# Performance work log

Hardware: AMD Instinct MI355X
Metric: run time of the kernel (lower is better)

## Reference

```python
import jax, jax.numpy as jnp
import numpy as np

B, CQ, CK, CV, CO = 16, 256, 256, 256, 256
H, W = 80, 80          # query spatial size (P3-like)
KH, KW = 40, 40        # key/value spatial size (P4-like)
HEADS = 4
R2 = 2 * 2             # region_size ** 2
SCALE = 1.0 / np.float32(np.sqrt(CQ))


def conv1x1(x, w, b):
    # 1x1 conv == per-pixel linear map over channels
    return jnp.einsum('bchw,oc->bohw', x, w) + b[None, :, None, None]


def setup_inputs() -> dict:
    key = jax.random.key(0)
    ks = jax.random.split(key, 10)
    s = 0.05
    return {
        'query': jax.random.normal(ks[0], (B, CQ, H, W), jnp.float32),
        'key':   jax.random.normal(ks[1], (B, CK, KH, KW), jnp.float32),
        'wq': jax.random.normal(ks[2], (CQ, CQ), jnp.float32) * s,
        'bq': jax.random.normal(ks[3], (CQ,), jnp.float32) * s,
        'wk': jax.random.normal(ks[4], (CK, CK), jnp.float32) * s,
        'bk': jax.random.normal(ks[5], (CK,), jnp.float32) * s,
        'wv': jax.random.normal(ks[6], (CV, CV), jnp.float32) * s,
        'bv': jax.random.normal(ks[7], (CV,), jnp.float32) * s,
        'wo': jax.random.normal(ks[8], (CO, CV), jnp.float32) * s,
        'bo': jax.random.normal(ks[9], (CO,), jnp.float32) * s,
    }


def reference(query, key, wq, bq, wk, bk, wv, bv, wo, bo):
    # value defaults to key in the original module
    q = conv1x1(query, wq, bq)               # [B,CQ,H,W]
    k = conv1x1(key, wk, bk)                 # [B,CK,KH,KW]
    v = conv1x1(key, wv, bv)                 # [B,CV,KH,KW]

    b, cq, h, w = q.shape
    # All R2 'patches' in the source are the SAME interpolation (no offsets),
    # so compute it once; bilinear resize matches torch align_corners=False.
    ki = jax.image.resize(k, (b, k.shape[1], h, w), method='bilinear')
    vi = jax.image.resize(v, (b, v.shape[1], h, w), method='bilinear')

    q5 = q.reshape(b, HEADS, cq // HEADS, h, w)
    k5 = ki.reshape(b, HEADS, k.shape[1] // HEADS, h, w)
    v5 = vi.reshape(b, HEADS, v.shape[1] // HEADS, h, w)

    # per-region score; identical for every region patch
    score = jnp.einsum('bhcxy,bhcxy->bhxy', q5, k5) * SCALE     # [B,h,H,W]
    scores = jnp.broadcast_to(score[:, :, None], (b, HEADS, R2, h, w))
    # NOTE: original uses nn.Softmax(dim=3) -> normalizes over the H axis
    attn = jax.nn.softmax(scores, axis=3)                       # [B,h,R2,H,W]

    # out = sum over regions of attn * v (v identical across regions)
    out = jnp.einsum('bhrxy,bhcxy->bhcxy', attn, v5)            # [B,h,C/h,H,W]
    out = out.reshape(b, -1, h, w)                              # [B,CV,H,W]
    return conv1x1(out, wo, bo)                                 # [B,CO,H,W]
```

## Files before the change

### kernel.cpp

```cpp
#include <hip/hip_runtime.h>
#include <hip/hip_bf16.h>

typedef __bf16 bf16;
typedef __attribute__((ext_vector_type(4))) float f32x4;
typedef __attribute__((ext_vector_type(8))) __bf16 bf16x8;
typedef __attribute__((ext_vector_type(4))) __bf16 bf16x4;

static __device__ __forceinline__ void gl16(const void* g, void* l) {
  __builtin_amdgcn_global_load_lds((const __attribute__((address_space(1))) void*)g,
                                   (__attribute__((address_space(3))) void*)l, 16, 0, 0);
}
static __device__ __forceinline__ bf16x8 frag(const bf16* tile, int row, int kb) {
  return *(const bf16x8*)(tile + row * 64 + ((((kb) >> 3) ^ (row & 7)) << 3));
}

__global__ void wpre(const float* __restrict__ w0, const float* __restrict__ w1,
                     const float* __restrict__ w2, const float* __restrict__ w3,
                     bf16* __restrict__ dst) {
  const float* srcs[4] = {w0, w1, w2, w3};
  const float* s = srcs[blockIdx.y];
  bf16* d = dst + (size_t)blockIdx.y * 65536;
  int base = blockIdx.x * 2048 + threadIdx.x * 8;
  f32x4 a = *(const f32x4*)(s + base);
  f32x4 b = *(const f32x4*)(s + base + 4);
  bf16x8 v = {(bf16)a[0], (bf16)a[1], (bf16)a[2], (bf16)a[3],
              (bf16)b[0], (bf16)b[1], (bf16)b[2], (bf16)b[3]};
  *(bf16x8*)(d + base) = v;
}

__global__ __launch_bounds__(256, 3)
void qscore(const float* __restrict__ query, const bf16* __restrict__ Wq,
            const float* __restrict__ bq, const bf16* __restrict__ Kpm,
            float* __restrict__ score) {
  __shared__ alignas(16) char smem[64 * 264 * 2];
  const int t = threadIdx.x;
  const int b = blockIdx.z;
  const int p0 = blockIdx.x * 64;
  const int w = t >> 6, l = t & 63;
  const int lrow = l & 15, ksel = l >> 4;
  const int pq = t & 15, cq = t >> 4;
  const float* actb = query + (size_t)b * 256 * 6400;

  auto Bt = [&](int buf) { return (bf16*)(smem + buf * 8192); };

  f32x4 Ar[4];
  auto ALOAD = [&](int kt) {
    const int k0 = kt * 64;
#pragma unroll
    for (int j = 0; j < 4; ++j)
      Ar[j] = *(const f32x4*)(actb + (size_t)(k0 + cq * 4 + j) * 6400 + p0 + pq * 4);
  };
  auto ASTORE = [&](int buf) {
    bf16* tile = Bt(buf);
#pragma unroll
    for (int e = 0; e < 4; ++e) {
      int row = pq * 4 + e;
      bf16x4 v = {(bf16)Ar[0][e], (bf16)Ar[1][e], (bf16)Ar[2][e], (bf16)Ar[3][e]};
      *(bf16x4*)(tile + row * 64 + ((((cq >> 1) ^ (row & 7)) << 3) | ((cq & 1) << 2))) = v;
    }
  };

  f32x4 acc[4][4];
#pragma unroll
  for (int i = 0; i < 4; ++i)
#pragma unroll
    for (int j = 0; j < 4; ++j) acc[i][j] = (f32x4){0.f, 0.f, 0.f, 0.f};

  auto COMPUTE = [&](int kt, int buf) {
    const int k0 = kt * 64;
    bf16x8 af[4][2];
#pragma unroll
    for (int mi = 0; mi < 4; ++mi)
#pragma unroll
      for (int kk = 0; kk < 2; ++kk)
        af[mi][kk] = *(const bf16x8*)(Wq + (size_t)(w * 64 + mi * 16 + lrow) * 256 +
                                      k0 + kk * 32 + ksel * 8);
    bf16x8 bv[4][2];
#pragma unroll
    for (int ni = 0; ni < 4; ++ni)
#pragma unroll
      for (int kk = 0; kk < 2; ++kk)
        bv[ni][kk] = frag(Bt(buf), ni * 16 + lrow, kk * 32 + ksel * 8);
#pragma unroll
    for (int kk = 0; kk < 2; ++kk)
#pragma unroll
      for (int mi = 0; mi < 4; ++mi)
#pragma unroll
        for (int ni = 0; ni < 4; ++ni)
          acc[mi][ni] = __builtin_amdgcn_mfma_f32_16x16x32_bf16(af[mi][kk], bv[ni][kk],
                                                                acc[mi][ni], 0, 0, 0);
  };

  ALOAD(0);
  ASTORE(0);
  __syncthreads();
#pragma unroll
  for (int kt = 0; kt < 4; ++kt) {
    if (kt < 3) ALOAD(kt + 1);
    COMPUTE(kt, kt & 1);
    if (kt < 3) ASTORE((kt + 1) & 1);
    __syncthreads();
  }

  __syncthreads();
  bf16* Qs = (bf16*)smem;
#pragma unroll
  for (int mi = 0; mi < 4; ++mi) {
#pragma unroll
    for (int r = 0; r < 4; ++r) {
      int o = w * 64 + mi * 16 + ksel * 4 + r;
      float bvf = bq[o];
#pragma unroll
      for (int ni = 0; ni < 4; ++ni) {
        int px = ni * 16 + lrow;
        Qs[px * 264 + o] = (bf16)(acc[mi][ni][r] + bvf);
      }
    }
  }
  __syncthreads();

  {
    int pl = t & 63, hd = t >> 6;
    int p = p0 + pl;
    int x = p / 80, y = p % 80;
    float cx = 0.5f * x - 0.25f;
    int ix = (int)floorf(cx);
    float wx1 = cx - ix;
    int x0 = ix < 0 ? 0 : ix, x1 = (ix + 1 > 39) ? 39 : ix + 1;
    float cy = 0.5f * y - 0.25f;
    int iy = (int)floorf(cy);
    float wy1 = cy - iy;
    int y0 = iy < 0 ? 0 : iy, y1 = (iy + 1 > 39) ? 39 : iy + 1;
    float w00 = (1.f - wx1) * (1.f - wy1), w01 = (1.f - wx1) * wy1;
    float w10 = wx1 * (1.f - wy1), w11 = wx1 * wy1;
    const bf16* k00 = Kpm + ((size_t)b * 1600 + x0 * 40 + y0) * 256 + hd * 64;
    const bf16* k01 = Kpm + ((size_t)b * 1600 + x0 * 40 + y1) * 256 + hd * 64;
    const bf16* k10 = Kpm + ((size_t)b * 1600 + x1 * 40 + y0) * 256 + hd * 64;
    const bf16* k11 = Kpm + ((size_t)b * 1600 + x1 * 40 + y1) * 256 + hd * 64;
    float dot = 0.f;
#pragma unroll
    for (int i = 0; i < 8; ++i) {
      bf16x8 qv = *(const bf16x8*)(Qs + pl * 264 + hd * 64 + i * 8);
      bf16x8 a = *(const bf16x8*)(k00 + i * 8);
      bf16x8 c = *(const bf16x8*)(k01 + i * 8);
      bf16x8 d = *(const bf16x8*)(k10 + i * 8);
      bf16x8 e = *(const bf16x8*)(k11 + i * 8);
#pragma unroll
      for (int j = 0; j < 8; ++j) {
        float kup = w00 * (float)a[j] + w01 * (float)c[j] + w10 * (float)d[j] + w11 * (float)e[j];
        dot += (float)qv[j] * kup;
      }
    }
    score[((size_t)b * 4 + hd) * 6400 + p] = dot * 0.0625f;
  }
}

__global__ __launch_bounds__(512, 1)
void kv_gemm(const float* __restrict__ key,
             const bf16* __restrict__ Wk, const float* __restrict__ bk, bf16* __restrict__ Kpm,
             const bf16* __restrict__ Wv, const float* __restrict__ bv, bf16* __restrict__ Vpm) {
  __shared__ alignas(16) char smem[65536];
  const int P = 1600;
  const int t = threadIdx.x;
  const int b = blockIdx.z;
  const int m0 = blockIdx.x * 128;
  const int sel = blockIdx.y >> 1;
  const int n0 = (blockIdx.y & 1) * 128;
  const bf16* W = sel ? Wv : Wk;
  const float* bias = sel ? bv : bk;
  bf16* out = sel ? Vpm : Kpm;
  const int w = t >> 6, l = t & 63;
  const int wr = w & 1, wc = w >> 1;
  const int lrow = l & 15, koff = (l >> 4) * 8;
  const int up = t & 31, uk = t >> 5;
  const float* actb = key + (size_t)b * 256 * P;

  f32x4 Ar[4];
  f32x4 acc[4][2];
#pragma unroll
  for (int i = 0; i < 4; ++i)
#pragma unroll
    for (int j = 0; j < 2; ++j) acc[i][j] = (f32x4){0.f, 0.f, 0.f, 0.f};

  auto Ab = [&](int buf) { return (bf16*)(smem + buf * 16384); };
  auto Bb = [&](int buf) { return (bf16*)(smem + 32768 + buf * 16384); };

  auto GLOADB = [&](int kt, int buf) {
    const int k0 = kt * 64;
#pragma unroll
    for (int call = 0; call < 2; ++call) {
      int idx = call * 512 + t;
      int row = idx >> 3, u = idx & 7;
      gl16(W + (size_t)(n0 + row) * 256 + k0 + ((u ^ (row & 7)) << 3), Bb(buf) + idx * 8);
    }
  };
  auto ALOAD = [&](int kt) {
    const int k0 = kt * 64;
    int ps = m0 + up * 4;
    if (ps > P - 4) ps = P - 4;
#pragma unroll
    for (int j = 0; j < 4; ++j)
      Ar[j] = *(const f32x4*)(actb + (size_t)(k0 + uk * 4 + j) * P + ps);
  };
  auto ASTORE = [&](int buf) {
#pragma unroll
    for (int j = 0; j < 4; ++j) {
      int row = up * 4 + j;
      int cs = (uk * 4) ^ ((row & 7) << 3);
      bf16x4 v = {(bf16)Ar[0][j], (bf16)Ar[1][j], (bf16)Ar[2][j], (bf16)Ar[3][j]};
      *(bf16x4*)(Ab(buf) + row * 64 + cs) = v;
    }
  };
  auto COMPUTE = [&](int buf) {
#pragma unroll
    for (int kk = 0; kk < 2; ++kk) {
      bf16x8 af[4], bvv[2];
      const int kb = kk * 32 + koff;
#pragma unroll
      for (int i = 0; i < 4; ++i) af[i] = frag(Ab(buf), wr * 64 + i * 16 + lrow, kb);
#pragma unroll
      for (int j = 0; j < 2; ++j) bvv[j] = frag(Bb(buf), wc * 32 + j * 16 + lrow, kb);
#pragma unroll
      for (int i = 0; i < 4; ++i)
#pragma unroll
        for (int j = 0; j < 2; ++j)
          acc[i][j] = __builtin_amdgcn_mfma_f32_16x16x32_bf16(af[i], bvv[j], acc[i][j], 0, 0, 0);
    }
  };

  GLOADB(0, 0);
  ALOAD(0);
  ASTORE(0);
  __syncthreads();
#pragma unroll
  for (int kt = 0; kt < 4; ++kt) {
    const int cur = kt & 1;
    if (kt < 3) { GLOADB(kt + 1, cur ^ 1); ALOAD(kt + 1); }
    __builtin_amdgcn_sched_barrier(0);
    COMPUTE(cur);
    if (kt < 3) ASTORE(cur ^ 1);
    __syncthreads();
  }

  bf16* Sc = (bf16*)smem;
#pragma unroll
  for (int mi = 0; mi < 4; ++mi) {
#pragma unroll
    for (int ni = 0; ni < 2; ++ni) {
      int ch = wc * 32 + ni * 16 + (l & 15);
      float bvf = bias[n0 + ch];
#pragma unroll
      for (int r = 0; r < 4; ++r) {
        int p = wr * 64 + mi * 16 + (l >> 4) * 4 + r;
        Sc[p * 136 + ch] = (bf16)(acc[mi][ni][r] + bvf);
      }
    }
  }
  __syncthreads();
  bf16* ob = out + (size_t)b * P * 256;
#pragma unroll
  for (int pass = 0; pass < 4; ++pass) {
    int unit = pass * 512 + t;
    int row = unit >> 4, cu = unit & 15;
    if (m0 + row < P) {
      bf16x8 v = *(const bf16x8*)(Sc + row * 136 + cu * 8);
      *(bf16x8*)(ob + (size_t)(m0 + row) * 256 + n0 + cu * 8) = v;
    }
  }
}

__global__ void smax_kernel(float* __restrict__ score) {
  __shared__ float s[6400];
  const int hd = blockIdx.x, b = blockIdx.y, t = threadIdx.x;
  float* buf = score + ((size_t)b * 4 + hd) * 6400;
  for (int i = t; i < 6400; i += 256) s[i] = buf[i];
  __syncthreads();
  if (t < 80) {
    const int y = t;
    float m = -1e30f;
    for (int x = 0; x < 80; ++x) m = fmaxf(m, s[x * 80 + y]);
    float sum = 0.f;
    for (int x = 0; x < 80; ++x) {
      float e = __expf(s[x * 80 + y] - m);
      s[x * 80 + y] = e;
      sum += e;
    }
    float inv = 4.0f / sum;
    for (int x = 0; x < 80; ++x) buf[x * 80 + y] = s[x * 80 + y] * inv;
  }
}

__global__ __launch_bounds__(256, 4)
void uv_gemm(const bf16* __restrict__ Vpm, const bf16* __restrict__ Wo,
             bf16* __restrict__ Uv) {
  __shared__ alignas(16) bf16 Vt[64 * 64];
  const int t = threadIdx.x;
  const int b = blockIdx.z;
  const int hd = blockIdx.y;
  const int q0 = blockIdx.x * 64;
  const int w = t >> 6, l = t & 63;
  const int lrow = l & 15, ksel = l >> 4;

  const bf16* vsrc = Vpm + ((size_t)b * 1600 + q0) * 256 + hd * 64;
#pragma unroll
  for (int call = 0; call < 2; ++call) {
    int idx = (w * 2 + call) * 64 + l;
    int q = idx >> 3, u = idx & 7;
    gl16(vsrc + (size_t)q * 256 + ((u ^ (q & 7)) << 3), Vt + idx * 8);
  }
  asm volatile("s_waitcnt vmcnt(0)" ::: "memory");
  __syncthreads();

  f32x4 acc[4][4];
#pragma unroll
  for (int i = 0; i < 4; ++i)
#pragma unroll
    for (int j = 0; j < 4; ++j) acc[i][j] = (f32x4){0.f, 0.f, 0.f, 0.f};

#pragma unroll
  for (int kk = 0; kk < 2; ++kk) {
    bf16x8 af[4], bv[4];
#pragma unroll
    for (int mi = 0; mi < 4; ++mi)
      af[mi] = *(const bf16x8*)(Wo + (size_t)(w * 64 + mi * 16 + lrow) * 256 +
                                hd * 64 + kk * 32 + ksel * 8);
#pragma unroll
    for (int ni = 0; ni < 4; ++ni)
      bv[ni] = frag(Vt, ni * 16 + lrow, kk * 32 + ksel * 8);
#pragma unroll
    for (int mi = 0; mi < 4; ++mi)
#pragma unroll
      for (int ni = 0; ni < 4; ++ni)
        acc[mi][ni] = __builtin_amdgcn_mfma_f32_16x16x32_bf16(af[mi], bv[ni], acc[mi][ni], 0, 0, 0);
  }

  bf16* ob = Uv + ((size_t)(b * 4 + hd)) * 256 * 1600;
#pragma unroll
  for (int mi = 0; mi < 4; ++mi) {
#pragma unroll
    for (int ni = 0; ni < 4; ++ni) {
#pragma unroll
      for (int r = 0; r < 4; ++r) {
        int o = w * 64 + mi * 16 + ksel * 4 + r;
        int q = q0 + ni * 16 + lrow;
        ob[(size_t)o * 1600 + q] = (bf16)acc[mi][ni][r];
      }
    }
  }
}

__global__ __launch_bounds__(256, 8)
void combine(const bf16* __restrict__ Uv, const float* __restrict__ attn,
             const float* __restrict__ bo, float* __restrict__ out) {
  __shared__ bf16 Us[4][1600];
  __shared__ int   sx0[80], sx1[80];
  __shared__ float swx[80];
  const int t = threadIdx.x;
  const int o = blockIdx.x;
  const int b = blockIdx.y;

  const bf16* usrc = Uv + (size_t)(b * 4) * 256 * 1600 + (size_t)o * 1600;
  for (int idx = t; idx < 800; idx += 256) {
    int hd = idx / 200, u = idx % 200;
    *(bf16x8*)&Us[hd][u * 8] = *(const bf16x8*)(usrc + (size_t)hd * 256 * 1600 + u * 8);
  }
  if (t < 80) {
    float c = 0.5f * t - 0.25f;
    int i0 = (int)floorf(c);
    swx[t] = c - i0;
    sx0[t] = i0 < 0 ? 0 : i0;
    sx1[t] = (i0 + 1 > 39) ? 39 : i0 + 1;
  }
  __syncthreads();

  const float bias = bo[o];
  const float* attb = attn + (size_t)b * 4 * 6400;
  float* op = out + ((size_t)b * 256 + o) * 6400;

  for (int p = t; p < 6400; p += 256) {
    int x = p / 80, y = p - x * 80;
    int x0 = sx0[x], x1 = sx1[x], y0 = sx0[y], y1 = sx1[y];
    float wx1 = swx[x], wy1 = swx[y];
    float w00 = (1.f - wx1) * (1.f - wy1), w01 = (1.f - wx1) * wy1;
    float w10 = wx1 * (1.f - wy1), w11 = wx1 * wy1;
    int q00 = x0 * 40 + y0, q01 = x0 * 40 + y1, q10 = x1 * 40 + y0, q11 = x1 * 40 + y1;
    float acc = bias;
#pragma unroll
    for (int hd = 0; hd < 4; ++hd) {
      float up = w00 * (float)Us[hd][q00] + w01 * (float)Us[hd][q01] +
                 w10 * (float)Us[hd][q10] + w11 * (float)Us[hd][q11];
      acc += attb[hd * 6400 + p] * up;
    }
    op[p] = acc;
  }
}

extern "C" void kernel_launch(void* const* d_in, const int* in_sizes, int n_in,
                              void* d_out, int out_size, void* d_ws, size_t ws_size,
                              hipStream_t stream) {
  const float* query = (const float*)d_in[0];
  const float* key   = (const float*)d_in[1];
  const float* wq    = (const float*)d_in[2];
  const float* bq    = (const float*)d_in[3];
  const float* wk    = (const float*)d_in[4];
  const float* bk    = (const float*)d_in[5];
  const float* wv    = (const float*)d_in[6];
  const float* bv    = (const float*)d_in[7];
  const float* wo    = (const float*)d_in[8];
  const float* bo    = (const float*)d_in[9];

  char* ws = (char*)d_ws;
  bf16*  Uv    = (bf16*)(ws);
  bf16*  Kpm   = (bf16*)(ws + 52428800);
  bf16*  Vpm   = (bf16*)(ws + 65536000);
  float* score = (float*)(ws + 78643200);
  bf16*  Wb    = (bf16*)(ws + 85196800);
  bf16* wqb = Wb, *wkb = Wb + 65536, *wvb = Wb + 131072, *wob = Wb + 196608;

  wpre<<<dim3(32, 4), 256, 0, stream>>>(wq, wk, wv, wo, Wb);
  kv_gemm<<<dim3(13, 4, 16), 512, 0, stream>>>(key, wkb, bk, Kpm, wvb, bv, Vpm);
  qscore<<<dim3(100, 1, 16), 256, 0, stream>>>(query, wqb, bq, Kpm, score);
  smax_kernel<<<dim3(4, 16), 256, 0, stream>>>(score);
  uv_gemm<<<dim3(25, 4, 16), 256, 0, stream>>>(Vpm, wob, Uv);
  combine<<<dim3(256, 16), 256, 0, stream>>>(Uv, score, bo, (float*)d_out);
}
```

Measured before the change: 170.6 us.

## Pre-transpose query and key to pixel-major bf16 for direct-to-LDS GEMM loads

Adds a transpose kernel that converts the fp32 channel-major query and key tensors into pixel-major bf16 buffers in scratch space (query into the Uv workspace region, key into the output buffer). The qscore and kv_gemm kernels then stage their activation tiles with asynchronous global-to-LDS 16-byte loads instead of register loads, conversion and swizzled LDS stores. This takes the conversion and scatter work out of the GEMM main loops, at the cost of two extra launches and an extra write and read of the activations. Reusing the output and Uv buffers as scratch depends on later kernels overwriting them in the right order.

```diff
diff --git a/kernel.cpp b/kernel.cpp
--- a/kernel.cpp
+++ b/kernel.cpp
@@ -28,8 +28,40 @@
   *(bf16x8*)(d + base) = v;
 }
 
+__global__ __launch_bounds__(256, 4)
+void tpose(const float* __restrict__ src, bf16* __restrict__ dst, int P) {
+  __shared__ bf16 tile[400][40];
+  const int t = threadIdx.x;
+  const int p0 = blockIdx.x * 400;
+  const int k0 = blockIdx.y * 32;
+  const int b = blockIdx.z;
+  const float* s = src + (size_t)b * 256 * P + (size_t)k0 * P + p0;
+  bf16* d = dst + (size_t)b * P * 256 + (size_t)p0 * 256 + k0;
+
+#pragma unroll
+  for (int pass = 0; pass < 13; ++pass) {
+    int idx = pass * 256 + t;
+    if (idx < 3200) {
+      int r = idx / 100, sg = idx - r * 100;
+      f32x4 v = *(const f32x4*)(s + (size_t)r * P + sg * 4);
+#pragma unroll
+      for (int j = 0; j < 4; ++j) tile[sg * 4 + j][r] = (bf16)v[j];
+    }
+  }
+  __syncthreads();
+#pragma unroll
+  for (int pass = 0; pass < 7; ++pass) {
+    int idx = pass * 256 + t;
+    if (idx < 1600) {
+      int row = idx >> 2, u = idx & 3;
+      bf16x8 v = *(const bf16x8*)&tile[row][u * 8];
+      *(bf16x8*)(d + (size_t)row * 256 + u * 8) = v;
+    }
+  }
+}
+
 __global__ __launch_bounds__(256, 3)
-void qscore(const float* __restrict__ query, const bf16* __restrict__ Wq,
+void qscore(const bf16* __restrict__ Qraw, const bf16* __restrict__ Wq,
             const float* __restrict__ bq, const bf16* __restrict__ Kpm,
             float* __restrict__ score) {
   __shared__ alignas(16) char smem[64 * 264 * 2];
@@ -38,25 +70,17 @@
   const int p0 = blockIdx.x * 64;
   const int w = t >> 6, l = t & 63;
   const int lrow = l & 15, ksel = l >> 4;
-  const int pq = t & 15, cq = t >> 4;
-  const float* actb = query + (size_t)b * 256 * 6400;
-
-  auto Bt = [&](int buf) { return (bf16*)(smem + buf * 8192); };
-
-  f32x4 Ar[4];
-  auto ALOAD = [&](int kt) {
+  const bf16* actb = Qraw + (size_t)b * 6400 * 256;
+
+  auto Ab = [&](int buf) { return (bf16*)(smem + buf * 8192); };
+
+  auto GLOADA = [&](int kt, int buf) {
     const int k0 = kt * 64;
 #pragma unroll
-    for (int j = 0; j < 4; ++j)
-      Ar[j] = *(const f32x4*)(actb + (size_t)(k0 + cq * 4 + j) * 6400 + p0 + pq * 4);
-  };
-  auto ASTORE = [&](int buf) {
-    bf16* tile = Bt(buf);
-#pragma unroll
-    for (int e = 0; e < 4; ++e) {
-      int row = pq * 4 + e;
-      bf16x4 v = {(bf16)Ar[0][e], (bf16)Ar[1][e], (bf16)Ar[2][e], (bf16)Ar[3][e]};
-      *(bf16x4*)(tile + row * 64 + ((((cq >> 1) ^ (row & 7)) << 3) | ((cq & 1) << 2))) = v;
+    for (int call = 0; call < 2; ++call) {
+      int idx = call * 256 + t;
+      int row = idx >> 3, u = idx & 7;
+      gl16(actb + (size_t)(p0 + row) * 256 + k0 + ((u ^ (row & 7)) << 3), Ab(buf) + idx * 8);
     }
   };
 
@@ -80,7 +104,7 @@
     for (int ni = 0; ni < 4; ++ni)
 #pragma unroll
       for (int kk = 0; kk < 2; ++kk)
-        bv[ni][kk] = frag(Bt(buf), ni * 16 + lrow, kk * 32 + ksel * 8);
+        bv[ni][kk] = frag(Ab(buf), ni * 16 + lrow, kk * 32 + ksel * 8);
 #pragma unroll
     for (int kk = 0; kk < 2; ++kk)
 #pragma unroll
@@ -91,18 +115,16 @@
                                                                 acc[mi][ni], 0, 0, 0);
   };
 
-  ALOAD(0);
-  ASTORE(0);
+  GLOADA(0, 0);
   __syncthreads();
 #pragma unroll
   for (int kt = 0; kt < 4; ++kt) {
-    if (kt < 3) ALOAD(kt + 1);
+    if (kt < 3) GLOADA(kt + 1, (kt + 1) & 1);
+    __builtin_amdgcn_sched_barrier(0);
     COMPUTE(kt, kt & 1);
-    if (kt < 3) ASTORE((kt + 1) & 1);
     __syncthreads();
   }
 
-  __syncthreads();
   bf16* Qs = (bf16*)smem;
 #pragma unroll
   for (int mi = 0; mi < 4; ++mi) {
@@ -156,7 +178,7 @@
 }
 
 __global__ __launch_bounds__(512, 1)
-void kv_gemm(const float* __restrict__ key,
+void kv_gemm(const bf16* __restrict__ Kraw,
              const bf16* __restrict__ Wk, const float* __restrict__ bk, bf16* __restrict__ Kpm,
              const bf16* __restrict__ Wv, const float* __restrict__ bv, bf16* __restrict__ Vpm) {
   __shared__ alignas(16) char smem[65536];
@@ -172,10 +194,8 @@
   const int w = t >> 6, l = t & 63;
   const int wr = w & 1, wc = w >> 1;
   const int lrow = l & 15, koff = (l >> 4) * 8;
-  const int up = t & 31, uk = t >> 5;
-  const float* actb = key + (size_t)b * 256 * P;
-
-  f32x4 Ar[4];
+  const bf16* actb = Kraw + (size_t)b * P * 256;
+
   f32x4 acc[4][2];
 #pragma unroll
   for (int i = 0; i < 4; ++i)
@@ -194,21 +214,14 @@
       gl16(W + (size_t)(n0 + row) * 256 + k0 + ((u ^ (row & 7)) << 3), Bb(buf) + idx * 8);
     }
   };
-  auto ALOAD = [&](int kt) {
+  auto GLOADA = [&](int kt, int buf) {
     const int k0 = kt * 64;
-    int ps = m0 + up * 4;
-    if (ps > P - 4) ps = P - 4;
-#pragma unroll
-    for (int j = 0; j < 4; ++j)
-      Ar[j] = *(const f32x4*)(actb + (size_t)(k0 + uk * 4 + j) * P + ps);
-  };
-  auto ASTORE = [&](int buf) {
-#pragma unroll
-    for (int j = 0; j < 4; ++j) {
-      int row = up * 4 + j;
-      int cs = (uk * 4) ^ ((row & 7) << 3);
-      bf16x4 v = {(bf16)Ar[0][j], (bf16)Ar[1][j], (bf16)Ar[2][j], (bf16)Ar[3][j]};
-      *(bf16x4*)(Ab(buf) + row * 64 + cs) = v;
+#pragma unroll
+    for (int call = 0; call < 2; ++call) {
+      int idx = call * 512 + t;
+      int row = idx >> 3, u = idx & 7;
+      int pr = m0 + row; if (pr > P - 1) pr = P - 1;
+      gl16(actb + (size_t)pr * 256 + k0 + ((u ^ (row & 7)) << 3), Ab(buf) + idx * 8);
     }
   };
   auto COMPUTE = [&](int buf) {
@@ -229,16 +242,14 @@
   };
 
   GLOADB(0, 0);
-  ALOAD(0);
-  ASTORE(0);
+  GLOADA(0, 0);
   __syncthreads();
 #pragma unroll
   for (int kt = 0; kt < 4; ++kt) {
     const int cur = kt & 1;
-    if (kt < 3) { GLOADB(kt + 1, cur ^ 1); ALOAD(kt + 1); }
+    if (kt < 3) { GLOADB(kt + 1, cur ^ 1); GLOADA(kt + 1, cur ^ 1); }
     __builtin_amdgcn_sched_barrier(0);
     COMPUTE(cur);
-    if (kt < 3) ASTORE(cur ^ 1);
     __syncthreads();
   }
 
@@ -410,16 +421,20 @@
   const float* bo    = (const float*)d_in[9];
 
   char* ws = (char*)d_ws;
+  bf16*  Qraw  = (bf16*)(ws);
   bf16*  Uv    = (bf16*)(ws);
   bf16*  Kpm   = (bf16*)(ws + 52428800);
   bf16*  Vpm   = (bf16*)(ws + 65536000);
   float* score = (float*)(ws + 78643200);
   bf16*  Wb    = (bf16*)(ws + 85196800);
   bf16* wqb = Wb, *wkb = Wb + 65536, *wvb = Wb + 131072, *wob = Wb + 196608;
+  bf16*  Kraw  = (bf16*)d_out;
 
   wpre<<<dim3(32, 4), 256, 0, stream>>>(wq, wk, wv, wo, Wb);
-  kv_gemm<<<dim3(13, 4, 16), 512, 0, stream>>>(key, wkb, bk, Kpm, wvb, bv, Vpm);
-  qscore<<<dim3(100, 1, 16), 256, 0, stream>>>(query, wqb, bq, Kpm, score);
+  tpose<<<dim3(16, 8, 16), 256, 0, stream>>>(query, Qraw, 6400);
+  tpose<<<dim3(4, 8, 16), 256, 0, stream>>>(key, Kraw, 1600);
+  kv_gemm<<<dim3(13, 4, 16), 512, 0, stream>>>(Kraw, wkb, bk, Kpm, wvb, bv, Vpm);
+  qscore<<<dim3(100, 1, 16), 256, 0, stream>>>(Qraw, wqb, bq, Kpm, score);
   smax_kernel<<<dim3(4, 16), 256, 0, stream>>>(score);
   uv_gemm<<<dim3(25, 4, 16), 256, 0, stream>>>(Vpm, wob, Uv);
   combine<<<dim3(256, 16), 256, 0, stream>>>(Uv, score, bo, (float*)d_out);
```

New measurement: 199.9 us. 17.2% more time.

## Load full activation K-range upfront and restructure KV projection as 64-pixel tiles

Applied to the files above, without the earlier changes.

The qscore kernel now issues all four K-chunk activation loads at once, stores them into four LDS tiles and syncs once, replacing the double-buffered loop with per-iteration barriers. The KV projection is rewritten in the same style: 64-pixel by 256-channel tiles, 256 threads, weights read straight from global memory, and a grid of 25x2x16. The goal is more memory-level parallelism and fewer synchronisations. The cost is higher register pressure, since launch bounds drop to 1 block per SM, and lower occupancy.

```diff
diff --git a/kernel.cpp b/kernel.cpp
--- a/kernel.cpp
+++ b/kernel.cpp
@@ -28,7 +28,7 @@
   *(bf16x8*)(d + base) = v;
 }
 
-__global__ __launch_bounds__(256, 3)
+__global__ __launch_bounds__(256, 1)
 void qscore(const float* __restrict__ query, const bf16* __restrict__ Wq,
             const float* __restrict__ bq, const bf16* __restrict__ Kpm,
             float* __restrict__ score) {
@@ -40,25 +40,25 @@
   const int lrow = l & 15, ksel = l >> 4;
   const int pq = t & 15, cq = t >> 4;
   const float* actb = query + (size_t)b * 256 * 6400;
-
-  auto Bt = [&](int buf) { return (bf16*)(smem + buf * 8192); };
-
-  f32x4 Ar[4];
-  auto ALOAD = [&](int kt) {
-    const int k0 = kt * 64;
+  bf16* As = (bf16*)smem;
+
+  f32x4 Ar[4][4];
+#pragma unroll
+  for (int kt = 0; kt < 4; ++kt)
 #pragma unroll
     for (int j = 0; j < 4; ++j)
-      Ar[j] = *(const f32x4*)(actb + (size_t)(k0 + cq * 4 + j) * 6400 + p0 + pq * 4);
-  };
-  auto ASTORE = [&](int buf) {
-    bf16* tile = Bt(buf);
+      Ar[kt][j] = *(const f32x4*)(actb + (size_t)(kt * 64 + cq * 4 + j) * 6400 + p0 + pq * 4);
+#pragma unroll
+  for (int kt = 0; kt < 4; ++kt) {
+    bf16* tile = As + kt * 4096;
 #pragma unroll
     for (int e = 0; e < 4; ++e) {
       int row = pq * 4 + e;
-      bf16x4 v = {(bf16)Ar[0][e], (bf16)Ar[1][e], (bf16)Ar[2][e], (bf16)Ar[3][e]};
+      bf16x4 v = {(bf16)Ar[kt][0][e], (bf16)Ar[kt][1][e], (bf16)Ar[kt][2][e], (bf16)Ar[kt][3][e]};
       *(bf16x4*)(tile + row * 64 + ((((cq >> 1) ^ (row & 7)) << 3) | ((cq & 1) << 2))) = v;
     }
-  };
+  }
+  __syncthreads();
 
   f32x4 acc[4][4];
 #pragma unroll
@@ -66,21 +66,22 @@
 #pragma unroll
     for (int j = 0; j < 4; ++j) acc[i][j] = (f32x4){0.f, 0.f, 0.f, 0.f};
 
-  auto COMPUTE = [&](int kt, int buf) {
+#pragma unroll
+  for (int kt = 0; kt < 4; ++kt) {
     const int k0 = kt * 64;
-    bf16x8 af[4][2];
+    const bf16* tile = As + kt * 4096;
+    bf16x8 af[4][2], bv[4][2];
 #pragma unroll
     for (int mi = 0; mi < 4; ++mi)
 #pragma unroll
       for (int kk = 0; kk < 2; ++kk)
         af[mi][kk] = *(const bf16x8*)(Wq + (size_t)(w * 64 + mi * 16 + lrow) * 256 +
                                       k0 + kk * 32 + ksel * 8);
-    bf16x8 bv[4][2];
 #pragma unroll
     for (int ni = 0; ni < 4; ++ni)
 #pragma unroll
       for (int kk = 0; kk < 2; ++kk)
-        bv[ni][kk] = frag(Bt(buf), ni * 16 + lrow, kk * 32 + ksel * 8);
+        bv[ni][kk] = frag(tile, ni * 16 + lrow, kk * 32 + ksel * 8);
 #pragma unroll
     for (int kk = 0; kk < 2; ++kk)
 #pragma unroll
@@ -89,20 +90,9 @@
         for (int ni = 0; ni < 4; ++ni)
           acc[mi][ni] = __builtin_amdgcn_mfma_f32_16x16x32_bf16(af[mi][kk], bv[ni][kk],
                                                                 acc[mi][ni], 0, 0, 0);
-  };
-
-  ALOAD(0);
-  ASTORE(0);
-  __syncthreads();
-#pragma unroll
-  for (int kt = 0; kt < 4; ++kt) {
-    if (kt < 3) ALOAD(kt + 1);
-    COMPUTE(kt, kt & 1);
-    if (kt < 3) ASTORE((kt + 1) & 1);
-    __syncthreads();
-  }
-
-  __syncthreads();
+  }
+  __syncthreads();
+
   bf16* Qs = (bf16*)smem;
 #pragma unroll
   for (int mi = 0; mi < 4; ++mi) {
@@ -155,117 +145,98 @@
   }
 }
 
-__global__ __launch_bounds__(512, 1)
-void kv_gemm(const float* __restrict__ key,
+__global__ __launch_bounds__(256, 1)
+void kv_proj(const float* __restrict__ key,
              const bf16* __restrict__ Wk, const float* __restrict__ bk, bf16* __restrict__ Kpm,
              const bf16* __restrict__ Wv, const float* __restrict__ bv, bf16* __restrict__ Vpm) {
-  __shared__ alignas(16) char smem[65536];
+  __shared__ alignas(16) char smem[64 * 264 * 2];
   const int P = 1600;
   const int t = threadIdx.x;
   const int b = blockIdx.z;
-  const int m0 = blockIdx.x * 128;
-  const int sel = blockIdx.y >> 1;
-  const int n0 = (blockIdx.y & 1) * 128;
+  const int p0 = blockIdx.x * 64;
+  const int sel = blockIdx.y;
   const bf16* W = sel ? Wv : Wk;
   const float* bias = sel ? bv : bk;
   bf16* out = sel ? Vpm : Kpm;
   const int w = t >> 6, l = t & 63;
-  const int wr = w & 1, wc = w >> 1;
-  const int lrow = l & 15, koff = (l >> 4) * 8;
-  const int up = t & 31, uk = t >> 5;
+  const int lrow = l & 15, ksel = l >> 4;
+  const int pq = t & 15, cq = t >> 4;
   const float* actb = key + (size_t)b * 256 * P;
-
-  f32x4 Ar[4];
-  f32x4 acc[4][2];
+  bf16* As = (bf16*)smem;
+
+  f32x4 Ar[4][4];
+#pragma unroll
+  for (int kt = 0; kt < 4; ++kt)
+#pragma unroll
+    for (int j = 0; j < 4; ++j)
+      Ar[kt][j] = *(const f32x4*)(actb + (size_t)(kt * 64 + cq * 4 + j) * P + p0 + pq * 4);
+#pragma unroll
+  for (int kt = 0; kt < 4; ++kt) {
+    bf16* tile = As + kt * 4096;
+#pragma unroll
+    for (int e = 0; e < 4; ++e) {
+      int row = pq * 4 + e;
+      bf16x4 v = {(bf16)Ar[kt][0][e], (bf16)Ar[kt][1][e], (bf16)Ar[kt][2][e], (bf16)Ar[kt][3][e]};
+      *(bf16x4*)(tile + row * 64 + ((((cq >> 1) ^ (row & 7)) << 3) | ((cq & 1) << 2))) = v;
+    }
+  }
+  __syncthreads();
+
+  f32x4 acc[4][4];
 #pragma unroll
   for (int i = 0; i < 4; ++i)
 #pragma unroll
-    for (int j = 0; j < 2; ++j) acc[i][j] = (f32x4){0.f, 0.f, 0.f, 0.f};
-
-  auto Ab = [&](int buf) { return (bf16*)(smem + buf * 16384); };
-  auto Bb = [&](int buf) { return (bf16*)(smem + 32768 + buf * 16384); };
-
-  auto GLOADB = [&](int kt, int buf) {
+    for (int j = 0; j < 4; ++j) acc[i][j] = (f32x4){0.f, 0.f, 0.f, 0.f};
+
+#pragma unroll
+  for (int kt = 0; kt < 4; ++kt) {
     const int k0 = kt * 64;
-#pragma unroll
-    for (int call = 0; call < 2; ++call) {
-      int idx = call * 512 + t;
-      int row = idx >> 3, u = idx & 7;
-      gl16(W + (size_t)(n0 + row) * 256 + k0 + ((u ^ (row & 7)) << 3), Bb(buf) + idx * 8);
-    }
-  };
-  auto ALOAD = [&](int kt) {
-    const int k0 = kt * 64;
-    int ps = m0 + up * 4;
-    if (ps > P - 4) ps = P - 4;
-#pragma unroll
-    for (int j = 0; j < 4; ++j)
-      Ar[j] = *(const f32x4*)(actb + (size_t)(k0 + uk * 4 + j) * P + ps);
-  };
-  auto ASTORE = [&](int buf) {
-#pragma unroll
-    for (int j = 0; j < 4; ++j) {
-      int row = up * 4 + j;
-      int cs = (uk * 4) ^ ((row & 7) << 3);
-      bf16x4 v = {(bf16)Ar[0][j], (bf16)Ar[1][j], (bf16)Ar[2][j], (bf16)Ar[3][j]};
-      *(bf16x4*)(Ab(buf) + row * 64 + cs) = v;
-    }
-  };
-  auto COMPUTE = [&](int buf) {
-#pragma unroll
-    for (int kk = 0; kk < 2; ++kk) {
-      bf16x8 af[4], bvv[2];
-      const int kb = kk * 32 + koff;
-#pragma unroll
-      for (int i = 0; i < 4; ++i) af[i] = frag(Ab(buf), wr * 64 + i * 16 + lrow, kb);
-#pragma unroll
-      for (int j = 0; j < 2; ++j) bvv[j] = frag(Bb(buf), wc * 32 + j * 16 + lrow, kb);
-#pragma unroll
-      for (int i = 0; i < 4; ++i)
-#pragma unroll
-        for (int j = 0; j < 2; ++j)
-          acc[i][j] = __builtin_amdgcn_mfma_f32_16x16x32_bf16(af[i], bvv[j], acc[i][j], 0, 0, 0);
-    }
-  };
-
-  GLOADB(0, 0);
-  ALOAD(0);
-  ASTORE(0);
-  __syncthreads();
-#pragma unroll
-  for (int kt = 0; kt < 4; ++kt) {
-    const int cur = kt & 1;
-    if (kt < 3) { GLOADB(kt + 1, cur ^ 1); ALOAD(kt + 1); }
-    __builtin_amdgcn_sched_barrier(0);
-    COMPUTE(cur);
-    if (kt < 3) ASTORE(cur ^ 1);
-    __syncthreads();
-  }
+    const bf16* tile = As + kt * 4096;
+    bf16x8 af[4][2], bv8[4][2];
+#pragma unroll
+    for (int mi = 0; mi < 4; ++mi)
+#pragma unroll
+      for (int kk = 0; kk < 2; ++kk)
+        af[mi][kk] = *(const bf16x8*)(W + (size_t)(w * 64 + mi * 16 + lrow) * 256 +
+                                      k0 + kk * 32 + ksel * 8);
+#pragma unroll
+    for (int ni = 0; ni < 4; ++ni)
+#pragma unroll
+      for (int kk = 0; kk < 2; ++kk)
+        bv8[ni][kk] = frag(tile, ni * 16 + lrow, kk * 32 + ksel * 8);
+#pragma unroll
+    for (int kk = 0; kk < 2; ++kk)
+#pragma unroll
+      for (int mi = 0; mi < 4; ++mi)
+#pragma unroll
+        for (int ni = 0; ni < 4; ++ni)
+          acc[mi][ni] = __builtin_amdgcn_mfma_f32_16x16x32_bf16(af[mi][kk], bv8[ni][kk],
+                                                                acc[mi][ni], 0, 0, 0);
+  }
+  __syncthreads();
 
   bf16* Sc = (bf16*)smem;
 #pragma unroll
   for (int mi = 0; mi < 4; ++mi) {
 #pragma unroll
-    for (int ni = 0; ni < 2; ++ni) {
-      int ch = wc * 32 + ni * 16 + (l & 15);
-      float bvf = bias[n0 + ch];
-#pragma unroll
-      for (int r = 0; r < 4; ++r) {
-        int p = wr * 64 + mi * 16 + (l >> 4) * 4 + r;
-        Sc[p * 136 + ch] = (bf16)(acc[mi][ni][r] + bvf);
+    for (int r = 0; r < 4; ++r) {
+      int o = w * 64 + mi * 16 + ksel * 4 + r;
+      float bvf = bias[o];
+#pragma unroll
+      for (int ni = 0; ni < 4; ++ni) {
+        int px = ni * 16 + lrow;
+        Sc[px * 264 + o] = (bf16)(acc[mi][ni][r] + bvf);
       }
     }
   }
   __syncthreads();
-  bf16* ob = out + (size_t)b * P * 256;
-#pragma unroll
-  for (int pass = 0; pass < 4; ++pass) {
-    int unit = pass * 512 + t;
-    int row = unit >> 4, cu = unit & 15;
-    if (m0 + row < P) {
-      bf16x8 v = *(const bf16x8*)(Sc + row * 136 + cu * 8);
-      *(bf16x8*)(ob + (size_t)(m0 + row) * 256 + n0 + cu * 8) = v;
-    }
+  bf16* ob = out + (size_t)b * P * 256 + (size_t)p0 * 256;
+#pragma unroll
+  for (int pass = 0; pass < 8; ++pass) {
+    int idx = pass * 256 + t;
+    int row = idx >> 5, cu = idx & 31;
+    bf16x8 v = *(const bf16x8*)(Sc + row * 264 + cu * 8);
+    *(bf16x8*)(ob + (size_t)row * 256 + cu * 8) = v;
   }
 }
 
@@ -418,7 +389,7 @@
   bf16* wqb = Wb, *wkb = Wb + 65536, *wvb = Wb + 131072, *wob = Wb + 196608;
 
   wpre<<<dim3(32, 4), 256, 0, stream>>>(wq, wk, wv, wo, Wb);
-  kv_gemm<<<dim3(13, 4, 16), 512, 0, stream>>>(key, wkb, bk, Kpm, wvb, bv, Vpm);
+  kv_proj<<<dim3(25, 2, 16), 256, 0, stream>>>(key, wkb, bk, Kpm, wvb, bv, Vpm);
   qscore<<<dim3(100, 1, 16), 256, 0, stream>>>(query, wqb, bq, Kpm, score);
   smax_kernel<<<dim3(4, 16), 256, 0, stream>>>(score);
   uv_gemm<<<dim3(25, 4, 16), 256, 0, stream>>>(Vpm, wob, Uv);
```

After: 179.9 us. +5.4%, slower.

## Merge uv_gemm into qscore launch and deepen query prefetch pipeline

Applied to the files above, without the earlier changes.

Folds the independent Uv GEMM blocks into the qscore kernel as extra blocks (blockIdx.x >= 100), removing one launch and letting the two workloads fill the GPU together. It also switches the qscore K-loop to two register buffers, so activation loads run two tiles ahead of compute. The cost is higher register pressure in the fused kernel, and the smaller uv blocks now run under qscore's launch bounds and shared-memory footprint.

```diff
diff --git a/kernel.cpp b/kernel.cpp
--- a/kernel.cpp
+++ b/kernel.cpp
@@ -29,28 +29,86 @@
 }
 
 __global__ __launch_bounds__(256, 3)
-void qscore(const float* __restrict__ query, const bf16* __restrict__ Wq,
-            const float* __restrict__ bq, const bf16* __restrict__ Kpm,
-            float* __restrict__ score) {
+void qscore_uv(const float* __restrict__ query, const bf16* __restrict__ Wq,
+               const float* __restrict__ bq, const bf16* __restrict__ Kpm,
+               float* __restrict__ score,
+               const bf16* __restrict__ Vpm, const bf16* __restrict__ Wo,
+               bf16* __restrict__ Uv) {
   __shared__ alignas(16) char smem[64 * 264 * 2];
   const int t = threadIdx.x;
-  const int b = blockIdx.z;
-  const int p0 = blockIdx.x * 64;
+  const int b = blockIdx.y;
   const int w = t >> 6, l = t & 63;
   const int lrow = l & 15, ksel = l >> 4;
+
+  if (blockIdx.x >= 100) {
+    const int u = blockIdx.x - 100;
+    const int q0 = (u % 25) * 64;
+    const int hd = u / 25;
+    bf16* Vt = (bf16*)smem;
+
+    const bf16* vsrc = Vpm + ((size_t)b * 1600 + q0) * 256 + hd * 64;
+#pragma unroll
+    for (int call = 0; call < 2; ++call) {
+      int idx = (w * 2 + call) * 64 + l;
+      int q = idx >> 3, uu = idx & 7;
+      gl16(vsrc + (size_t)q * 256 + ((uu ^ (q & 7)) << 3), Vt + idx * 8);
+    }
+    asm volatile("s_waitcnt vmcnt(0)" ::: "memory");
+    __syncthreads();
+
+    f32x4 acc[4][4];
+#pragma unroll
+    for (int i = 0; i < 4; ++i)
+#pragma unroll
+      for (int j = 0; j < 4; ++j) acc[i][j] = (f32x4){0.f, 0.f, 0.f, 0.f};
+
+#pragma unroll
+    for (int kk = 0; kk < 2; ++kk) {
+      bf16x8 af[4], bv[4];
+#pragma unroll
+      for (int mi = 0; mi < 4; ++mi)
+        af[mi] = *(const bf16x8*)(Wo + (size_t)(w * 64 + mi * 16 + lrow) * 256 +
+                                  hd * 64 + kk * 32 + ksel * 8);
+#pragma unroll
+      for (int ni = 0; ni < 4; ++ni)
+        bv[ni] = frag(Vt, ni * 16 + lrow, kk * 32 + ksel * 8);
+#pragma unroll
+      for (int mi = 0; mi < 4; ++mi)
+#pragma unroll
+        for (int ni = 0; ni < 4; ++ni)
+          acc[mi][ni] = __builtin_amdgcn_mfma_f32_16x16x32_bf16(af[mi], bv[ni], acc[mi][ni], 0, 0, 0);
+    }
+
+    bf16* ob = Uv + ((size_t)(b * 4 + hd)) * 256 * 1600;
+#pragma unroll
+    for (int mi = 0; mi < 4; ++mi) {
+#pragma unroll
+      for (int ni = 0; ni < 4; ++ni) {
+#pragma unroll
+        for (int r = 0; r < 4; ++r) {
+          int o = w * 64 + mi * 16 + ksel * 4 + r;
+          int q = q0 + ni * 16 + lrow;
+          ob[(size_t)o * 1600 + q] = (bf16)acc[mi][ni][r];
+        }
+      }
+    }
+    return;
+  }
+
+  const int p0 = blockIdx.x * 64;
   const int pq = t & 15, cq = t >> 4;
   const float* actb = query + (size_t)b * 256 * 6400;
 
   auto Bt = [&](int buf) { return (bf16*)(smem + buf * 8192); };
 
-  f32x4 Ar[4];
-  auto ALOAD = [&](int kt) {
+  f32x4 ArA[4], ArB[4];
+  auto ALOAD = [&](int kt, f32x4* Ar) {
     const int k0 = kt * 64;
 #pragma unroll
     for (int j = 0; j < 4; ++j)
       Ar[j] = *(const f32x4*)(actb + (size_t)(k0 + cq * 4 + j) * 6400 + p0 + pq * 4);
   };
-  auto ASTORE = [&](int buf) {
+  auto ASTORE = [&](const f32x4* Ar, int buf) {
     bf16* tile = Bt(buf);
 #pragma unroll
     for (int e = 0; e < 4; ++e) {
@@ -91,18 +149,24 @@
                                                                 acc[mi][ni], 0, 0, 0);
   };
 
-  ALOAD(0);
-  ASTORE(0);
-  __syncthreads();
-#pragma unroll
-  for (int kt = 0; kt < 4; ++kt) {
-    if (kt < 3) ALOAD(kt + 1);
-    COMPUTE(kt, kt & 1);
-    if (kt < 3) ASTORE((kt + 1) & 1);
-    __syncthreads();
-  }
-
-  __syncthreads();
+  ALOAD(0, ArA);
+  ASTORE(ArA, 0);
+  ALOAD(1, ArB);
+  __syncthreads();
+  ALOAD(2, ArA);
+  COMPUTE(0, 0);
+  ASTORE(ArB, 1);
+  __syncthreads();
+  ALOAD(3, ArB);
+  COMPUTE(1, 1);
+  ASTORE(ArA, 0);
+  __syncthreads();
+  COMPUTE(2, 0);
+  ASTORE(ArB, 1);
+  __syncthreads();
+  COMPUTE(3, 1);
+  __syncthreads();
+
   bf16* Qs = (bf16*)smem;
 #pragma unroll
   for (int mi = 0; mi < 4; ++mi) {
@@ -290,65 +354,6 @@
   }
 }
 
-__global__ __launch_bounds__(256, 4)
-void uv_gemm(const bf16* __restrict__ Vpm, const bf16* __restrict__ Wo,
-             bf16* __restrict__ Uv) {
-  __shared__ alignas(16) bf16 Vt[64 * 64];
-  const int t = threadIdx.x;
-  const int b = blockIdx.z;
-  const int hd = blockIdx.y;
-  const int q0 = blockIdx.x * 64;
-  const int w = t >> 6, l = t & 63;
-  const int lrow = l & 15, ksel = l >> 4;
-
-  const bf16* vsrc = Vpm + ((size_t)b * 1600 + q0) * 256 + hd * 64;
-#pragma unroll
-  for (int call = 0; call < 2; ++call) {
-    int idx = (w * 2 + call) * 64 + l;
-    int q = idx >> 3, u = idx & 7;
-    gl16(vsrc + (size_t)q * 256 + ((u ^ (q & 7)) << 3), Vt + idx * 8);
-  }
-  asm volatile("s_waitcnt vmcnt(0)" ::: "memory");
-  __syncthreads();
-
-  f32x4 acc[4][4];
-#pragma unroll
-  for (int i = 0; i < 4; ++i)
-#pragma unroll
-    for (int j = 0; j < 4; ++j) acc[i][j] = (f32x4){0.f, 0.f, 0.f, 0.f};
-
-#pragma unroll
-  for (int kk = 0; kk < 2; ++kk) {
-    bf16x8 af[4], bv[4];
-#pragma unroll
-    for (int mi = 0; mi < 4; ++mi)
-      af[mi] = *(const bf16x8*)(Wo + (size_t)(w * 64 + mi * 16 + lrow) * 256 +
-                                hd * 64 + kk * 32 + ksel * 8);
-#pragma unroll
-    for (int ni = 0; ni < 4; ++ni)
-      bv[ni] = frag(Vt, ni * 16 + lrow, kk * 32 + ksel * 8);
-#pragma unroll
-    for (int mi = 0; mi < 4; ++mi)
-#pragma unroll
-      for (int ni = 0; ni < 4; ++ni)
-        acc[mi][ni] = __builtin_amdgcn_mfma_f32_16x16x32_bf16(af[mi], bv[ni], acc[mi][ni], 0, 0, 0);
-  }
-
-  bf16* ob = Uv + ((size_t)(b * 4 + hd)) * 256 * 1600;
-#pragma unroll
-  for (int mi = 0; mi < 4; ++mi) {
-#pragma unroll
-    for (int ni = 0; ni < 4; ++ni) {
-#pragma unroll
-      for (int r = 0; r < 4; ++r) {
-        int o = w * 64 + mi * 16 + ksel * 4 + r;
-        int q = q0 + ni * 16 + lrow;
-        ob[(size_t)o * 1600 + q] = (bf16)acc[mi][ni][r];
-      }
-    }
-  }
-}
-
 __global__ __launch_bounds__(256, 8)
 void combine(const bf16* __restrict__ Uv, const float* __restrict__ attn,
              const float* __restrict__ bo, float* __restrict__ out) {
@@ -419,8 +424,7 @@
 
   wpre<<<dim3(32, 4), 256, 0, stream>>>(wq, wk, wv, wo, Wb);
   kv_gemm<<<dim3(13, 4, 16), 512, 0, stream>>>(key, wkb, bk, Kpm, wvb, bv, Vpm);
-  qscore<<<dim3(100, 1, 16), 256, 0, stream>>>(query, wqb, bq, Kpm, score);
+  qscore_uv<<<dim3(200, 16), 256, 0, stream>>>(query, wqb, bq, Kpm, score, Vpm, wob, Uv);
   smax_kernel<<<dim3(4, 16), 256, 0, stream>>>(score);
-  uv_gemm<<<dim3(25, 4, 16), 256, 0, stream>>>(Vpm, wob, Uv);
   combine<<<dim3(256, 16), 256, 0, stream>>>(Uv, score, bo, (float*)d_out);
 }
```

After: 170.9 us. About the same (+0.1%).
